# Optimization experiments

Hardware: AMD Instinct MI355X
Metric: run time of the kernel (lower is better)

## Reference

```python
import jax, jax.numpy as jnp
import numpy as np

DIM = 1024
NUM_HEADS = 16
HEAD_DIM = DIM // NUM_HEADS
EPS = 1e-6


def rmsnorm(x, scale):
    # normalize over last dim (head_dim)
    ms = jnp.mean(x * x, axis=-1, keepdims=True)
    return scale * (x * jax.lax.rsqrt(ms + EPS))


def setup_inputs() -> dict:
    key = jax.random.key(0)
    ks = jax.random.split(key, 12)
    B, Nx, Nc = 2, 2048, 256
    std = 1.0 / np.sqrt(DIM)
    return {
        "x": jax.random.normal(ks[0], (B, Nx, DIM), jnp.float32),
        "c": jax.random.normal(ks[1], (B, Nc, DIM), jnp.float32),
        "w_qkv_x": jax.random.normal(ks[2], (DIM, 3 * DIM), jnp.float32) * std,
        "b_qkv_x": jnp.zeros((3 * DIM,), jnp.float32),
        "w_qkv_c": jax.random.normal(ks[3], (DIM, 3 * DIM), jnp.float32) * std,
        "b_qkv_c": jnp.zeros((3 * DIM,), jnp.float32),
        "s_q_x": jnp.ones((HEAD_DIM,), jnp.float32),
        "s_k_x": jnp.ones((HEAD_DIM,), jnp.float32),
        "s_q_c": jnp.ones((HEAD_DIM,), jnp.float32),
        "s_k_c": jnp.ones((HEAD_DIM,), jnp.float32),
        "w_proj_x": jax.random.normal(ks[4], (DIM, DIM), jnp.float32) * std,
        "b_proj_x": jnp.zeros((DIM,), jnp.float32),
        "w_proj_c": jax.random.normal(ks[5], (DIM, DIM), jnp.float32) * std,
        "b_proj_c": jnp.zeros((DIM,), jnp.float32),
    }


def reference(x, c, w_qkv_x, b_qkv_x, w_qkv_c, b_qkv_c,
              s_q_x, s_k_x, s_q_c, s_k_c,
              w_proj_x, b_proj_x, w_proj_c, b_proj_c):
    B, Nx, C = x.shape
    Nc = c.shape[1]
    H, D = NUM_HEADS, HEAD_DIM

    def split_qkv(t, w, b, n):
        qkv = (t @ w + b).reshape(B, n, 3, H, D)
        qkv = jnp.transpose(qkv, (2, 0, 3, 1, 4))  # [3, B, H, n, D]
        return qkv[0], qkv[1], qkv[2]

    q_x, k_x, v_x = split_qkv(x, w_qkv_x, b_qkv_x, Nx)
    q_c, k_c, v_c = split_qkv(c, w_qkv_c, b_qkv_c, Nc)

    q = jnp.concatenate([rmsnorm(q_x, s_q_x), rmsnorm(q_c, s_q_c)], axis=2)
    k = jnp.concatenate([rmsnorm(k_x, s_k_x), rmsnorm(k_c, s_k_c)], axis=2)
    v = jnp.concatenate([v_x, v_c], axis=2)

    scale = 1.0 / jnp.sqrt(jnp.asarray(D, q.dtype))
    scores = jnp.einsum("bhqd,bhkd->bhqk", q, k) * scale
    attn = jax.nn.softmax(scores, axis=-1)
    out = jnp.einsum("bhqk,bhkd->bhqd", attn, v)  # [B, H, Nx+Nc, D]
    out = jnp.transpose(out, (0, 2, 1, 3)).reshape(B, Nx + Nc, C)

    x_out = out[:, :Nx] @ w_proj_x + b_proj_x
    c_out = out[:, Nx:] @ w_proj_c + b_proj_c
    return x_out, c_out
```

## Files before the change

kernel.cpp:

```cpp
#include <hip/hip_runtime.h>
#include <stdint.h>

typedef __attribute__((ext_vector_type(4))) float  f32x4;
typedef __attribute__((ext_vector_type(2))) float  f32x2;
typedef __attribute__((ext_vector_type(8))) short  s16x8;
typedef __attribute__((ext_vector_type(4))) short  s16x4;

constexpr int kDIM = 1024;
constexpr int kD   = 64;
constexpr int kNT  = 2304;

static __device__ __forceinline__ short f2bf(float f) {
  union { float f; uint32_t i; } x; x.f = f;
  uint32_t r = x.i + 0x7fffu + ((x.i >> 16) & 1u);
  return (short)(r >> 16);
}
static __device__ __forceinline__ uint32_t cvtpk(float lo, float hi) {
  uint32_t r;
  asm volatile("v_cvt_pk_bf16_f32 %0, %1, %2" : "=v"(r) : "v"(lo), "v"(hi));
  return r;
}
static __device__ __forceinline__ void gll16(const short* g, short* l) {
  __builtin_amdgcn_global_load_lds((const __attribute__((address_space(1))) void*)g,
                                   (__attribute__((address_space(3))) void*)l, 16, 0, 0);
}
#define FENCE() asm volatile("" ::: "memory")
#define WAITV8() asm volatile("s_waitcnt vmcnt(8)" ::: "memory")
#define WAITV2() asm volatile("s_waitcnt vmcnt(2)" ::: "memory")
#define WAITV0() asm volatile("s_waitcnt vmcnt(0)" ::: "memory")
#define WAITLGKM() do { asm volatile("s_waitcnt lgkmcnt(0)" ::: "memory"); \
                        __builtin_amdgcn_sched_barrier(0); } while (0)

__global__ __launch_bounds__(256) void k_cast2(const float* __restrict__ x,
                                               short* __restrict__ xb,
                                               const float* __restrict__ c,
                                               short* __restrict__ cb, int nxb) {
  int b = blockIdx.x;
  const float* in = x; short* out = xb;
  if (b >= nxb) { in = c; out = cb; b -= nxb; }
  int i = (b * 256 + threadIdx.x) * 4;
  f32x4 v = *(const f32x4*)(in + i);
  s16x4 o; o[0] = f2bf(v[0]); o[1] = f2bf(v[1]); o[2] = f2bf(v[2]); o[3] = f2bf(v[3]);
  *(s16x4*)(out + i) = o;
}

__global__ __launch_bounds__(256) void k_tcast2(const float* __restrict__ W0,
                                                short* __restrict__ Wt0,
                                                const float* __restrict__ W1,
                                                short* __restrict__ Wt1,
                                                int K, int N) {
  const float* W = blockIdx.z ? W1 : W0;
  short* Wt = blockIdx.z ? Wt1 : Wt0;
  __shared__ float tile[32][33];
  int n0 = blockIdx.x * 32, k0 = blockIdx.y * 32;
  int tx = threadIdx.x, ty = threadIdx.y;
#pragma unroll
  for (int i2 = 0; i2 < 4; ++i2) {
    int r = ty + 8 * i2;
    tile[r][tx] = W[(size_t)(k0 + r) * N + n0 + tx];
  }
  __syncthreads();
#pragma unroll
  for (int i2 = 0; i2 < 4; ++i2) {
    int r = ty + 8 * i2;
    Wt[(size_t)(n0 + r) * K + k0 + tx] = f2bf(tile[tx][r]);
  }
}

__global__ __launch_bounds__(256, 2) void k_gemm(
    const short* A0, const short* Wt0, const float* bias0,
    const float* sq0, const float* sk0,
    const short* A1, const short* Wt1, const float* bias1,
    const float* sq1, const float* sk1,
    short* outq, short* outk, short* outvt,
    float* outp0, float* outp1,
    int rpbs0, int arstride0, int aoff0, int posoff0,
    int rpbs1, int arstride1, int aoff1, int posoff1,
    int ybreak, int epi, int nx) {
  __shared__ __align__(16) short SH[32768];
  short* As0 = SH;          short* As1 = SH + 8192;
  short* Bs0 = SH + 16384;  short* Bs1 = SH + 24576;
  const int t = threadIdx.x;
  const int lane = t & 63, w = t >> 6;
  const int g = lane >> 4, r15 = lane & 15;
  const int wm = w >> 1, wn = w & 1;

  int lin = blockIdx.x;
  int xcd = lin & 7, kk = lin >> 3;
  int by = (xcd & 3) * 9 + kk % 9;
  int bx = (xcd >> 2) * (nx >> 1) + kk / 9;

  const short* A; const short* Wt; const float* bias;
  const float* sq; const float* sk; float* outp;
  int rpbs, arstride, aoff, posoff, my;
  if (by < ybreak) {
    A = A0; Wt = Wt0; bias = bias0; sq = sq0; sk = sk0; outp = outp0;
    rpbs = rpbs0; arstride = arstride0; aoff = aoff0; posoff = posoff0; my = by;
  } else {
    A = A1; Wt = Wt1; bias = bias1; sq = sq1; sk = sk1; outp = outp1;
    rpbs = rpbs1; arstride = arstride1; aoff = aoff1; posoff = posoff1; my = by - ybreak;
  }
  const int m0 = my * 128, n0 = bx * 128;

  const short* aptr[4]; const short* bptr[4];
  int wofs[4];
#pragma unroll
  for (int it = 0; it < 4; ++it) {
    int slot = t + 256 * it;
    int row = slot >> 3, gp = slot & 7;
    int gl = gp ^ (row & 7);
    int i = m0 + row;
    int arow = (i >> rpbs) * arstride + aoff + (i & ((1 << rpbs) - 1));
    aptr[it] = A + (size_t)arow * kDIM + 8 * gl;
    bptr[it] = Wt + (size_t)(n0 + row) * kDIM + 8 * gl;
    wofs[it] = (256 * it + 64 * w) * 8;
  }

  f32x4 acc[4][4] = {};

  auto STAGE = [&](short* Asd, short* Bsd) {
#pragma unroll
    for (int it = 0; it < 4; ++it) {
      gll16(aptr[it], Asd + wofs[it]);
      gll16(bptr[it], Bsd + wofs[it]);
      aptr[it] += 64; bptr[it] += 64;
    }
  };

  auto kstep = [&](const short* Ab, const short* Bb, short* Asd, short* Bsd,
                   bool last, bool pref) {
    if (last) WAITV0(); else WAITV8();
    __builtin_amdgcn_s_barrier();
    FENCE();
#pragma unroll
    for (int ks = 0; ks < 2; ++ks) {
      s16x8 af[4], bfr[4];
#pragma unroll
      for (int mf = 0; mf < 4; ++mf) {
        int row = wm * 64 + mf * 16 + r15;
        af[mf] = *(const s16x8*)(Ab + row * 64 + (((g + 4 * ks) ^ (row & 7)) * 8));
      }
#pragma unroll
      for (int nf = 0; nf < 4; ++nf) {
        int row = wn * 64 + nf * 16 + r15;
        bfr[nf] = *(const s16x8*)(Bb + row * 64 + (((g + 4 * ks) ^ (row & 7)) * 8));
      }
#pragma unroll
      for (int mf = 0; mf < 4; ++mf)
#pragma unroll
        for (int nf = 0; nf < 4; ++nf)
          acc[mf][nf] = __builtin_amdgcn_mfma_f32_16x16x32_bf16(af[mf], bfr[nf], acc[mf][nf], 0, 0, 0);
    }
    FENCE();
    __builtin_amdgcn_s_barrier();
    FENCE();
    if (pref) STAGE(Asd, Bsd);
  };

  STAGE(As0, Bs0);
  STAGE(As1, Bs1);
  for (int pp = 0; pp < 8; ++pp) {
    kstep(As0, Bs0, As0, Bs0, false,   pp < 7);
    kstep(As1, Bs1, As1, Bs1, pp == 7, pp < 7);
  }

  const int rpbm = (1 << rpbs) - 1;
  float* Ep = (float*)SH + w * 4096;

  if (epi == 1) {
#pragma unroll
    for (int mf = 0; mf < 4; ++mf)
#pragma unroll
      for (int nf = 0; nf < 4; ++nf) {
        f32x4 v = acc[mf][nf];
        float bj = bias[n0 + wn * 64 + nf * 16 + r15];
        int dl = nf * 16 + r15;
#pragma unroll
        for (int rg = 0; rg < 4; ++rg) {
          int r = mf * 16 + 4 * g + rg;
          Ep[r * 64 + (dl ^ ((r & 15) << 1))] = v[rg] + bj;
        }
      }
    WAITLGKM();
#pragma unroll
    for (int p2 = 0; p2 < 16; ++p2) {
      int r = 4 * p2 + (lane >> 4);
      int ch = lane & 15;
      int i = m0 + wm * 64 + r;
      f32x2 a = *(const f32x2*)&Ep[r * 64 + ((ch * 4) ^ ((r & 15) << 1))];
      f32x2 b2 = *(const f32x2*)&Ep[r * 64 + ((ch * 4 + 2) ^ ((r & 15) << 1))];
      f32x4 o; o[0] = a[0]; o[1] = a[1]; o[2] = b2[0]; o[3] = b2[1];
      *(f32x4*)(outp + (size_t)i * 1024 + n0 + wn * 64 + ch * 4) = o;
    }
    return;
  }

  const int eblk = (n0 + wn * 64) >> 10;
  const int hh = ((n0 + wn * 64) >> 6) & 15;
  if (eblk == 2) {
#pragma unroll
    for (int mf = 0; mf < 4; ++mf)
#pragma unroll
      for (int nf = 0; nf < 4; ++nf) {
        f32x4 v = acc[mf][nf];
        float bj = bias[n0 + wn * 64 + nf * 16 + r15];
        int dl = nf * 16 + r15;
#pragma unroll
        for (int rg = 0; rg < 4; ++rg) {
          int pin = mf * 16 + 4 * g + rg;
          int pp2 = (pin & 32) | (((pin >> 2) & 3) << 3) |
                    (((pin >> 4) & 1) << 2) | (pin & 3);
          Ep[dl * 64 + (pp2 ^ ((dl & 15) << 1))] = v[rg] + bj;
        }
      }
    WAITLGKM();
    int i0 = m0 + wm * 64;
    int b = i0 >> rpbs;
    int posb = (i0 & rpbm) + posoff;
#pragma unroll
    for (int p2 = 0; p2 < 8; ++p2) {
      int dl = 8 * p2 + (lane >> 3);
      int ch = lane & 7;
      union { uint32_t u[4]; s16x8 v; } o;
#pragma unroll
      for (int j = 0; j < 4; ++j) {
        f32x2 rd = *(const f32x2*)&Ep[dl * 64 + ((ch * 8 + 2 * j) ^ ((dl & 15) << 1))];
        o.u[j] = cvtpk(rd[0], rd[1]);
      }
      *(s16x8*)(outvt + ((size_t)((b * 16 + hh) * 64 + dl)) * kNT + posb + ch * 8) = o.v;
    }
  } else {
    const float* sv = (eblk == 0) ? sq : sk;
    short* dstb = (eblk == 0) ? outq : outk;
    const float post = (eblk == 0) ? 0.125f * 1.44269504f : 1.0f;
    float sl[4], bj4[4];
#pragma unroll
    for (int nf = 0; nf < 4; ++nf) {
      bj4[nf] = bias[n0 + wn * 64 + nf * 16 + r15];
      sl[nf] = sv[nf * 16 + r15] * post;
    }
#pragma unroll
    for (int mf = 0; mf < 4; ++mf) {
      float vb[4][4];
#pragma unroll
      for (int nf = 0; nf < 4; ++nf)
#pragma unroll
        for (int rg = 0; rg < 4; ++rg)
          vb[nf][rg] = acc[mf][nf][rg] + bj4[nf];
#pragma unroll
      for (int rg = 0; rg < 4; ++rg) {
        float ss = vb[0][rg] * vb[0][rg];
        ss = __builtin_fmaf(vb[1][rg], vb[1][rg], ss);
        ss = __builtin_fmaf(vb[2][rg], vb[2][rg], ss);
        ss = __builtin_fmaf(vb[3][rg], vb[3][rg], ss);
        ss += __shfl_xor(ss, 1); ss += __shfl_xor(ss, 2);
        ss += __shfl_xor(ss, 4); ss += __shfl_xor(ss, 8);
        float f = rsqrtf(ss * (1.f / 64.f) + 1e-6f);
        int r = mf * 16 + 4 * g + rg;
#pragma unroll
        for (int nf = 0; nf < 4; ++nf) {
          int dl = nf * 16 + r15;
          Ep[r * 64 + (dl ^ ((r & 15) << 1))] = vb[nf][rg] * f * sl[nf];
        }
      }
    }
    WAITLGKM();
#pragma unroll
    for (int p2 = 0; p2 < 8; ++p2) {
      int r = 8 * p2 + (lane >> 3);
      int ch = lane & 7;
      int i = m0 + wm * 64 + r;
      int b = i >> rpbs;
      int pos = (i & rpbm) + posoff;
      union { uint32_t u[4]; s16x8 v; } o;
#pragma unroll
      for (int j = 0; j < 4; ++j) {
        f32x2 rd = *(const f32x2*)&Ep[r * 64 + ((ch * 8 + 2 * j) ^ ((r & 15) << 1))];
        o.u[j] = cvtpk(rd[0], rd[1]);
      }
      *(s16x8*)(dstb + ((size_t)((b * 16 + hh) * kNT + pos)) * 64 + ch * 8) = o.v;
    }
  }
}

__global__ __launch_bounds__(512, 4) void k_attn(
    const short* __restrict__ Q, const short* __restrict__ K,
    const short* __restrict__ Vt, short* __restrict__ Ao) {
  __shared__ __align__(16) short S[16384];
  const int t = threadIdx.x;
  const int lane = t & 63, w = t >> 6;
  const int g = lane >> 4, r15 = lane & 15;
  const int lin = blockIdx.x;
  const int idx = lin >> 3;
  const int bh = (lin & 7) * 4 + idx / 18;
  const int q0 = (idx % 18) * 128;

  const short* qrow = Q + ((size_t)bh * kNT + q0 + 16 * w + r15) * kD;
  s16x8 qf0 = *(const s16x8*)(qrow + 8 * g);
  s16x8 qf1 = *(const s16x8*)(qrow + 32 + 8 * g);

  {
  }
  int srow = t >> 3, sgp = t & 7;
  int sgl = sgp ^ (srow & 7);
  const short* kptr = K + ((size_t)bh * kNT + srow) * kD + 8 * sgl;
  const short* vptr = Vt + ((size_t)bh * kD + srow) * kNT + 8 * sgl;
  const int sb2 = 512 * w;

  int ko[2][4], vo[2][4];
#pragma unroll
  for (int a = 0; a < 2; ++a)
#pragma unroll
    for (int rf = 0; rf < 4; ++rf) {
      int row = 16 * rf + r15;
      ko[a][rf] = row * 64 + (((g + 4 * a) ^ (row & 7)) * 8);
      vo[a][rf] = row * 64 + (((4 * a + g) ^ (row & 7)) * 8);
    }

  s16x8 onesf;
#pragma unroll
  for (int j = 0; j < 8; ++j) onesf[j] = (short)0x3F80;

  f32x4 ot[4] = {};
  f32x4 ls = {};
  short* Kb0 = S;          short* Kb1 = S + 4096;
  short* Vb0 = S + 8192;   short* Vb1 = S + 12288;

  auto STAGE = [&](short* kst, short* vst) {
    gll16(kptr, kst + sb2); kptr += 64 * kD;
    gll16(vptr, vst + sb2); vptr += 64;
  };

  auto tile = [&](const short* Kb, const short* Vb, short* kst, short* vst,
                  bool last, bool pref) {
    if (last) WAITV0(); else WAITV2();
    __builtin_amdgcn_s_barrier();
    FENCE();
    f32x4 st[4] = {};
    __builtin_amdgcn_s_setprio(1);
#pragma unroll
    for (int a = 0; a < 2; ++a) {
      s16x8 qk = a ? qf1 : qf0;
#pragma unroll
      for (int rf = 0; rf < 4; ++rf) {
        s16x8 kf = *(const s16x8*)(Kb + ko[a][rf]);
        st[rf] = __builtin_amdgcn_mfma_f32_16x16x32_bf16(kf, qk, st[rf], 0, 0, 0);
      }
    }
    __builtin_amdgcn_s_setprio(0);
    float pv[4][4];
#pragma unroll
    for (int rf = 0; rf < 4; ++rf)
#pragma unroll
      for (int j = 0; j < 4; ++j)
        pv[rf][j] = __builtin_amdgcn_exp2f(st[rf][j]);
    s16x8 pf[2];
#pragma unroll
    for (int c = 0; c < 2; ++c) {
      union { uint32_t u[4]; s16x8 v; } pk;
      pk.u[0] = cvtpk(pv[2 * c][0], pv[2 * c][1]);
      pk.u[1] = cvtpk(pv[2 * c][2], pv[2 * c][3]);
      pk.u[2] = cvtpk(pv[2 * c + 1][0], pv[2 * c + 1][1]);
      pk.u[3] = cvtpk(pv[2 * c + 1][2], pv[2 * c + 1][3]);
      pf[c] = pk.v;
    }
    __builtin_amdgcn_s_setprio(1);
#pragma unroll
    for (int mf = 0; mf < 4; ++mf)
#pragma unroll
      for (int c = 0; c < 2; ++c) {
        s16x8 vf = *(const s16x8*)(Vb + vo[c][mf]);
        ot[mf] = __builtin_amdgcn_mfma_f32_16x16x32_bf16(vf, pf[c], ot[mf], 0, 0, 0);
      }
#pragma unroll
    for (int c = 0; c < 2; ++c)
      ls = __builtin_amdgcn_mfma_f32_16x16x32_bf16(onesf, pf[c], ls, 0, 0, 0);
    __builtin_amdgcn_s_setprio(0);
    FENCE();
    __builtin_amdgcn_s_barrier();
    FENCE();
    if (pref) STAGE(kst, vst);
  };

  STAGE(Kb0, Vb0);
  STAGE(Kb1, Vb1);
  for (int pp = 0; pp < 18; ++pp) {
    tile(Kb0, Vb0, Kb0, Vb0, false,    pp < 17);
    tile(Kb1, Vb1, Kb1, Vb1, pp == 17, pp < 17);
  }

  float rl = 1.f / ls[0];

  __syncthreads();
  float* Os = (float*)S;
#pragma unroll
  for (int mf = 0; mf < 4; ++mf)
#pragma unroll
    for (int rg = 0; rg < 4; ++rg) {
      int d = 16 * mf + 4 * g + rg;
      int R = 16 * w + r15;
      Os[R * 64 + (d ^ ((r15 & 7) << 3))] = ot[mf][rg] * rl;
    }
  __syncthreads();
  {
    int b = bh >> 4, h = bh & 15;
    int q = t >> 2, c4 = t & 3;
    float vals[16];
#pragma unroll
    for (int i = 0; i < 4; ++i) {
      f32x4 rd = *(const f32x4*)&Os[q * 64 + (((c4 * 16 + 4 * i) ^ ((q & 7) << 3)))];
      vals[4 * i + 0] = rd[0]; vals[4 * i + 1] = rd[1];
      vals[4 * i + 2] = rd[2]; vals[4 * i + 3] = rd[3];
    }
    union { uint32_t u[4]; s16x8 v; } o0, o1;
    o0.u[0] = cvtpk(vals[0], vals[1]);   o0.u[1] = cvtpk(vals[2], vals[3]);
    o0.u[2] = cvtpk(vals[4], vals[5]);   o0.u[3] = cvtpk(vals[6], vals[7]);
    o1.u[0] = cvtpk(vals[8], vals[9]);   o1.u[1] = cvtpk(vals[10], vals[11]);
    o1.u[2] = cvtpk(vals[12], vals[13]); o1.u[3] = cvtpk(vals[14], vals[15]);
    short* dst = Ao + ((size_t)b * kNT + q0 + q) * kDIM + h * kD + c4 * 16;
    *(s16x8*)dst = o0.v;
    *(s16x8*)(dst + 8) = o1.v;
  }
}

extern "C" void kernel_launch(void* const* d_in, const int* in_sizes, int n_in,
                              void* d_out, int out_size, void* d_ws, size_t ws_size,
                              hipStream_t stream) {
  const float* x   = (const float*)d_in[0];
  const float* c   = (const float*)d_in[1];
  const float* wqx = (const float*)d_in[2];
  const float* bqx = (const float*)d_in[3];
  const float* wqc = (const float*)d_in[4];
  const float* bqc = (const float*)d_in[5];
  const float* sqx = (const float*)d_in[6];
  const float* skx = (const float*)d_in[7];
  const float* sqc = (const float*)d_in[8];
  const float* skc = (const float*)d_in[9];
  const float* wpx = (const float*)d_in[10];
  const float* bpx = (const float*)d_in[11];
  const float* wpc = (const float*)d_in[12];
  const float* bpc = (const float*)d_in[13];
  float* out = (float*)d_out;

  char* p = (char*)d_ws;
  short* xb   = (short*)p; p += (size_t)4096 * 1024 * 2;
  short* cb   = (short*)p; p += (size_t)512 * 1024 * 2;
  short* wqxt = (short*)p; p += (size_t)3072 * 1024 * 2;
  short* wqct = (short*)p; p += (size_t)3072 * 1024 * 2;
  short* wpxt = (short*)p; p += (size_t)1024 * 1024 * 2;
  short* wpct = (short*)p; p += (size_t)1024 * 1024 * 2;
  short* qb   = (short*)p; p += (size_t)32 * 2304 * 64 * 2;
  short* kb   = (short*)p; p += (size_t)32 * 2304 * 64 * 2;
  short* vtb  = (short*)p; p += (size_t)32 * 64 * 2304 * 2;
  short* ao   = (short*)p; p += (size_t)2 * 2304 * 1024 * 2;

  k_cast2<<<4608, 256, 0, stream>>>(x, xb, c, cb, 4096);
  k_tcast2<<<dim3(96, 32, 2), dim3(32, 8), 0, stream>>>(wqx, wqxt, wqc, wqct, 1024, 3072);
  k_tcast2<<<dim3(32, 32, 2), dim3(32, 8), 0, stream>>>(wpx, wpxt, wpc, wpct, 1024, 1024);

  k_gemm<<<864, 256, 0, stream>>>(
      xb, wqxt, bqx, sqx, skx,
      cb, wqct, bqc, sqc, skc,
      qb, kb, vtb, nullptr, nullptr,
      11, 2048, 0, 0,
      8, 256, 0, 2048,
      32, 0, 24);

  k_attn<<<576, 512, 0, stream>>>(qb, kb, vtb, ao);

  k_gemm<<<288, 256, 0, stream>>>(
      ao, wpxt, bpx, nullptr, nullptr,
      ao, wpct, bpc, nullptr, nullptr,
      nullptr, nullptr, nullptr, out, out + (size_t)4096 * 1024,
      11, 2304, 0, 0,
      8, 2304, 2048, 0,
      32, 1, 8);
}
```

Measured before the change: 130.1 us.

## Give each attention wave four query fragments and shrink blocks to two waves

The attention kernel now runs 128-thread blocks where each wave handles 64 query rows (four 16-row fragments) instead of 16. Each K/V fragment read from shared memory is reused across four MFMAs, and the staging loop issues four loads per thread to fill the same tiles. This cuts LDS traffic per MFMA and barrier overhead per unit of work. In exchange it raises register pressure from the larger accumulators and leaves far fewer waves per CU to hide latency. The vmcnt wait is adjusted to match the larger number of in-flight loads.

```diff
diff --git a/kernel.cpp b/kernel.cpp
--- a/kernel.cpp
+++ b/kernel.cpp
@@ -26,7 +26,6 @@
 }
 #define FENCE() asm volatile("" ::: "memory")
 #define WAITV8() asm volatile("s_waitcnt vmcnt(8)" ::: "memory")
-#define WAITV2() asm volatile("s_waitcnt vmcnt(2)" ::: "memory")
 #define WAITV0() asm volatile("s_waitcnt vmcnt(0)" ::: "memory")
 #define WAITLGKM() do { asm volatile("s_waitcnt lgkmcnt(0)" ::: "memory"); \
                         __builtin_amdgcn_sched_barrier(0); } while (0)
@@ -283,7 +282,7 @@
   }
 }
 
-__global__ __launch_bounds__(512, 4) void k_attn(
+__global__ __launch_bounds__(128, 2) void k_attn(
     const short* __restrict__ Q, const short* __restrict__ K,
     const short* __restrict__ Vt, short* __restrict__ Ao) {
   __shared__ __align__(16) short S[16384];
@@ -295,17 +294,25 @@
   const int bh = (lin & 7) * 4 + idx / 18;
   const int q0 = (idx % 18) * 128;
 
-  const short* qrow = Q + ((size_t)bh * kNT + q0 + 16 * w + r15) * kD;
-  s16x8 qf0 = *(const s16x8*)(qrow + 8 * g);
-  s16x8 qf1 = *(const s16x8*)(qrow + 32 + 8 * g);
-
-  {
-  }
-  int srow = t >> 3, sgp = t & 7;
-  int sgl = sgp ^ (srow & 7);
-  const short* kptr = K + ((size_t)bh * kNT + srow) * kD + 8 * sgl;
-  const short* vptr = Vt + ((size_t)bh * kD + srow) * kNT + 8 * sgl;
-  const int sb2 = 512 * w;
+  s16x8 qf[4][2];
+#pragma unroll
+  for (int qi = 0; qi < 4; ++qi) {
+    const short* qrow = Q + ((size_t)bh * kNT + q0 + 64 * w + 16 * qi + r15) * kD;
+    qf[qi][0] = *(const s16x8*)(qrow + 8 * g);
+    qf[qi][1] = *(const s16x8*)(qrow + 32 + 8 * g);
+  }
+
+  const short* kptr[4]; const short* vptr[4];
+  int sb[4];
+#pragma unroll
+  for (int it = 0; it < 4; ++it) {
+    int slot = lane + 64 * (2 * it + w);
+    int row = slot >> 3, gp = slot & 7;
+    int gl = gp ^ (row & 7);
+    kptr[it] = K + ((size_t)bh * kNT + row) * kD + 8 * gl;
+    vptr[it] = Vt + ((size_t)bh * kD + row) * kNT + 8 * gl;
+    sb[it] = 512 * (2 * it + w);
+  }
 
   int ko[2][4], vo[2][4];
 #pragma unroll
@@ -321,60 +328,72 @@
 #pragma unroll
   for (int j = 0; j < 8; ++j) onesf[j] = (short)0x3F80;
 
-  f32x4 ot[4] = {};
-  f32x4 ls = {};
+  f32x4 ot[4][4] = {};
+  f32x4 ls[4] = {};
   short* Kb0 = S;          short* Kb1 = S + 4096;
   short* Vb0 = S + 8192;   short* Vb1 = S + 12288;
 
   auto STAGE = [&](short* kst, short* vst) {
-    gll16(kptr, kst + sb2); kptr += 64 * kD;
-    gll16(vptr, vst + sb2); vptr += 64;
+#pragma unroll
+    for (int it = 0; it < 4; ++it) {
+      gll16(kptr[it], kst + sb[it]); kptr[it] += 64 * kD;
+      gll16(vptr[it], vst + sb[it]); vptr[it] += 64;
+    }
   };
 
   auto tile = [&](const short* Kb, const short* Vb, short* kst, short* vst,
                   bool last, bool pref) {
-    if (last) WAITV0(); else WAITV2();
+    if (last) WAITV0(); else WAITV8();
     __builtin_amdgcn_s_barrier();
     FENCE();
-    f32x4 st[4] = {};
+    f32x4 st[4][4];
     __builtin_amdgcn_s_setprio(1);
 #pragma unroll
-    for (int a = 0; a < 2; ++a) {
-      s16x8 qk = a ? qf1 : qf0;
+    for (int a = 0; a < 2; ++a)
 #pragma unroll
       for (int rf = 0; rf < 4; ++rf) {
         s16x8 kf = *(const s16x8*)(Kb + ko[a][rf]);
-        st[rf] = __builtin_amdgcn_mfma_f32_16x16x32_bf16(kf, qk, st[rf], 0, 0, 0);
-      }
-    }
+#pragma unroll
+        for (int qi = 0; qi < 4; ++qi) {
+          if (a == 0) st[qi][rf] = __builtin_amdgcn_mfma_f32_16x16x32_bf16(kf, qf[qi][0], f32x4{}, 0, 0, 0);
+          else        st[qi][rf] = __builtin_amdgcn_mfma_f32_16x16x32_bf16(kf, qf[qi][1], st[qi][rf], 0, 0, 0);
+        }
+      }
     __builtin_amdgcn_s_setprio(0);
-    float pv[4][4];
-#pragma unroll
-    for (int rf = 0; rf < 4; ++rf)
-#pragma unroll
-      for (int j = 0; j < 4; ++j)
-        pv[rf][j] = __builtin_amdgcn_exp2f(st[rf][j]);
-    s16x8 pf[2];
-#pragma unroll
-    for (int c = 0; c < 2; ++c) {
-      union { uint32_t u[4]; s16x8 v; } pk;
-      pk.u[0] = cvtpk(pv[2 * c][0], pv[2 * c][1]);
-      pk.u[1] = cvtpk(pv[2 * c][2], pv[2 * c][3]);
-      pk.u[2] = cvtpk(pv[2 * c + 1][0], pv[2 * c + 1][1]);
-      pk.u[3] = cvtpk(pv[2 * c + 1][2], pv[2 * c + 1][3]);
-      pf[c] = pk.v;
+    s16x8 pf[4][2];
+#pragma unroll
+    for (int qi = 0; qi < 4; ++qi) {
+      float pv[4][4];
+#pragma unroll
+      for (int rf = 0; rf < 4; ++rf)
+#pragma unroll
+        for (int j = 0; j < 4; ++j)
+          pv[rf][j] = __builtin_amdgcn_exp2f(st[qi][rf][j]);
+#pragma unroll
+      for (int c = 0; c < 2; ++c) {
+        union { uint32_t u[4]; s16x8 v; } pk;
+        pk.u[0] = cvtpk(pv[2 * c][0], pv[2 * c][1]);
+        pk.u[1] = cvtpk(pv[2 * c][2], pv[2 * c][3]);
+        pk.u[2] = cvtpk(pv[2 * c + 1][0], pv[2 * c + 1][1]);
+        pk.u[3] = cvtpk(pv[2 * c + 1][2], pv[2 * c + 1][3]);
+        pf[qi][c] = pk.v;
+      }
     }
     __builtin_amdgcn_s_setprio(1);
 #pragma unroll
-    for (int mf = 0; mf < 4; ++mf)
-#pragma unroll
-      for (int c = 0; c < 2; ++c) {
+    for (int c = 0; c < 2; ++c)
+#pragma unroll
+      for (int mf = 0; mf < 4; ++mf) {
         s16x8 vf = *(const s16x8*)(Vb + vo[c][mf]);
-        ot[mf] = __builtin_amdgcn_mfma_f32_16x16x32_bf16(vf, pf[c], ot[mf], 0, 0, 0);
+#pragma unroll
+        for (int qi = 0; qi < 4; ++qi)
+          ot[qi][mf] = __builtin_amdgcn_mfma_f32_16x16x32_bf16(vf, pf[qi][c], ot[qi][mf], 0, 0, 0);
       }
 #pragma unroll
     for (int c = 0; c < 2; ++c)
-      ls = __builtin_amdgcn_mfma_f32_16x16x32_bf16(onesf, pf[c], ls, 0, 0, 0);
+#pragma unroll
+      for (int qi = 0; qi < 4; ++qi)
+        ls[qi] = __builtin_amdgcn_mfma_f32_16x16x32_bf16(onesf, pf[qi][c], ls[qi], 0, 0, 0);
     __builtin_amdgcn_s_setprio(0);
     FENCE();
     __builtin_amdgcn_s_barrier();
@@ -389,37 +408,45 @@
     tile(Kb1, Vb1, Kb1, Vb1, pp == 17, pp < 17);
   }
 
-  float rl = 1.f / ls[0];
+  float rl[4];
+#pragma unroll
+  for (int qi = 0; qi < 4; ++qi) rl[qi] = 1.f / ls[qi][0];
 
   __syncthreads();
   float* Os = (float*)S;
 #pragma unroll
-  for (int mf = 0; mf < 4; ++mf)
-#pragma unroll
-    for (int rg = 0; rg < 4; ++rg) {
-      int d = 16 * mf + 4 * g + rg;
-      int R = 16 * w + r15;
-      Os[R * 64 + (d ^ ((r15 & 7) << 3))] = ot[mf][rg] * rl;
-    }
+  for (int qi = 0; qi < 4; ++qi)
+#pragma unroll
+    for (int mf = 0; mf < 4; ++mf)
+#pragma unroll
+      for (int rg = 0; rg < 4; ++rg) {
+        int d = 16 * mf + 4 * g + rg;
+        int R = 64 * w + 16 * qi + r15;
+        Os[R * 64 + (d ^ ((r15 & 7) << 3))] = ot[qi][mf][rg] * rl[qi];
+      }
   __syncthreads();
   {
     int b = bh >> 4, h = bh & 15;
-    int q = t >> 2, c4 = t & 3;
-    float vals[16];
-#pragma unroll
-    for (int i = 0; i < 4; ++i) {
-      f32x4 rd = *(const f32x4*)&Os[q * 64 + (((c4 * 16 + 4 * i) ^ ((q & 7) << 3)))];
-      vals[4 * i + 0] = rd[0]; vals[4 * i + 1] = rd[1];
-      vals[4 * i + 2] = rd[2]; vals[4 * i + 3] = rd[3];
-    }
-    union { uint32_t u[4]; s16x8 v; } o0, o1;
-    o0.u[0] = cvtpk(vals[0], vals[1]);   o0.u[1] = cvtpk(vals[2], vals[3]);
-    o0.u[2] = cvtpk(vals[4], vals[5]);   o0.u[3] = cvtpk(vals[6], vals[7]);
-    o1.u[0] = cvtpk(vals[8], vals[9]);   o1.u[1] = cvtpk(vals[10], vals[11]);
-    o1.u[2] = cvtpk(vals[12], vals[13]); o1.u[3] = cvtpk(vals[14], vals[15]);
-    short* dst = Ao + ((size_t)b * kNT + q0 + q) * kDIM + h * kD + c4 * 16;
-    *(s16x8*)dst = o0.v;
-    *(s16x8*)(dst + 8) = o1.v;
+#pragma unroll
+    for (int rep = 0; rep < 4; ++rep) {
+      int idx2 = t + 128 * rep;
+      int q = idx2 >> 2, c4 = idx2 & 3;
+      float vals[16];
+#pragma unroll
+      for (int i = 0; i < 4; ++i) {
+        f32x4 rd = *(const f32x4*)&Os[q * 64 + (((c4 * 16 + 4 * i) ^ ((q & 7) << 3)))];
+        vals[4 * i + 0] = rd[0]; vals[4 * i + 1] = rd[1];
+        vals[4 * i + 2] = rd[2]; vals[4 * i + 3] = rd[3];
+      }
+      union { uint32_t u[4]; s16x8 v; } o0, o1;
+      o0.u[0] = cvtpk(vals[0], vals[1]);   o0.u[1] = cvtpk(vals[2], vals[3]);
+      o0.u[2] = cvtpk(vals[4], vals[5]);   o0.u[3] = cvtpk(vals[6], vals[7]);
+      o1.u[0] = cvtpk(vals[8], vals[9]);   o1.u[1] = cvtpk(vals[10], vals[11]);
+      o1.u[2] = cvtpk(vals[12], vals[13]); o1.u[3] = cvtpk(vals[14], vals[15]);
+      short* dst = Ao + ((size_t)b * kNT + q0 + q) * kDIM + h * kD + c4 * 16;
+      *(s16x8*)dst = o0.v;
+      *(s16x8*)(dst + 8) = o1.v;
+    }
   }
 }
 
@@ -466,7 +493,7 @@
       8, 256, 0, 2048,
       32, 0, 24);
 
-  k_attn<<<576, 512, 0, stream>>>(qb, kb, vtb, ao);
+  k_attn<<<576, 128, 0, stream>>>(qb, kb, vtb, ao);
 
   k_gemm<<<288, 256, 0, stream>>>(
       ao, wpxt, bpx, nullptr, nullptr,
```

Result: slower. 138.3 us (+6.2%).

## Switch attention kernel to 32x32x16 MFMA with 256-thread blocks

Applied to the files above, without the earlier changes.

Rewrites the attention inner loop to use 32x32x16 bf16 MFMA instructions, with each wave owning 32 query rows, and halves the block to 256 threads, so each thread now stages two K/V chunks per tile. The row sum is now built with scalar adds plus a cross-lane shuffle, replacing the extra ones-vector MFMA. The bit permutation in the GEMM epilogue is also simplified. The aim is fewer MFMA issues and LDS fragment reads per unit of work, at the cost of larger accumulator register use and fewer waves per block to hide latency.

```diff
diff --git a/kernel.cpp b/kernel.cpp
--- a/kernel.cpp
+++ b/kernel.cpp
@@ -1,10 +1,11 @@
 #include <hip/hip_runtime.h>
 #include <stdint.h>
 
-typedef __attribute__((ext_vector_type(4))) float  f32x4;
-typedef __attribute__((ext_vector_type(2))) float  f32x2;
-typedef __attribute__((ext_vector_type(8))) short  s16x8;
-typedef __attribute__((ext_vector_type(4))) short  s16x4;
+typedef __attribute__((ext_vector_type(4)))  float f32x4;
+typedef __attribute__((ext_vector_type(2)))  float f32x2;
+typedef __attribute__((ext_vector_type(16))) float f32x16;
+typedef __attribute__((ext_vector_type(8)))  short s16x8;
+typedef __attribute__((ext_vector_type(4)))  short s16x4;
 
 constexpr int kDIM = 1024;
 constexpr int kD   = 64;
@@ -26,7 +27,7 @@
 }
 #define FENCE() asm volatile("" ::: "memory")
 #define WAITV8() asm volatile("s_waitcnt vmcnt(8)" ::: "memory")
-#define WAITV2() asm volatile("s_waitcnt vmcnt(2)" ::: "memory")
+#define WAITV4() asm volatile("s_waitcnt vmcnt(4)" ::: "memory")
 #define WAITV0() asm volatile("s_waitcnt vmcnt(0)" ::: "memory")
 #define WAITLGKM() do { asm volatile("s_waitcnt lgkmcnt(0)" ::: "memory"); \
                         __builtin_amdgcn_sched_barrier(0); } while (0)
@@ -208,8 +209,7 @@
 #pragma unroll
         for (int rg = 0; rg < 4; ++rg) {
           int pin = mf * 16 + 4 * g + rg;
-          int pp2 = (pin & 32) | (((pin >> 2) & 3) << 3) |
-                    (((pin >> 4) & 1) << 2) | (pin & 3);
+          int pp2 = (pin & 51) | ((pin & 4) << 1) | ((pin & 8) >> 1);
           Ep[dl * 64 + (pp2 ^ ((dl & 15) << 1))] = v[rg] + bj;
         }
       }
@@ -283,98 +283,104 @@
   }
 }
 
-__global__ __launch_bounds__(512, 4) void k_attn(
+__global__ __launch_bounds__(256, 3) void k_attn(
     const short* __restrict__ Q, const short* __restrict__ K,
     const short* __restrict__ Vt, short* __restrict__ Ao) {
   __shared__ __align__(16) short S[16384];
   const int t = threadIdx.x;
   const int lane = t & 63, w = t >> 6;
-  const int g = lane >> 4, r15 = lane & 15;
+  const int h = lane >> 5, q31 = lane & 31;
   const int lin = blockIdx.x;
   const int idx = lin >> 3;
   const int bh = (lin & 7) * 4 + idx / 18;
   const int q0 = (idx % 18) * 128;
 
-  const short* qrow = Q + ((size_t)bh * kNT + q0 + 16 * w + r15) * kD;
-  s16x8 qf0 = *(const s16x8*)(qrow + 8 * g);
-  s16x8 qf1 = *(const s16x8*)(qrow + 32 + 8 * g);
-
-  {
-  }
-  int srow = t >> 3, sgp = t & 7;
-  int sgl = sgp ^ (srow & 7);
-  const short* kptr = K + ((size_t)bh * kNT + srow) * kD + 8 * sgl;
-  const short* vptr = Vt + ((size_t)bh * kD + srow) * kNT + 8 * sgl;
-  const int sb2 = 512 * w;
+  const short* qrow = Q + ((size_t)bh * kNT + q0 + 32 * w + q31) * kD;
+  s16x8 qf[4];
+#pragma unroll
+  for (int a = 0; a < 4; ++a)
+    qf[a] = *(const s16x8*)(qrow + 16 * a + 8 * h);
+
+  const short* kptr[2]; const short* vptr[2];
+  int sb[2];
+#pragma unroll
+  for (int it = 0; it < 2; ++it) {
+    int slot = t + 256 * it;
+    int row = slot >> 3, gp = slot & 7;
+    int gl = gp ^ (row & 7);
+    kptr[it] = K + ((size_t)bh * kNT + row) * kD + 8 * gl;
+    vptr[it] = Vt + ((size_t)bh * kD + row) * kNT + 8 * gl;
+    sb[it] = (256 * it + 64 * w) * 8;
+  }
 
   int ko[2][4], vo[2][4];
 #pragma unroll
-  for (int a = 0; a < 2; ++a)
-#pragma unroll
-    for (int rf = 0; rf < 4; ++rf) {
-      int row = 16 * rf + r15;
-      ko[a][rf] = row * 64 + (((g + 4 * a) ^ (row & 7)) * 8);
-      vo[a][rf] = row * 64 + (((4 * a + g) ^ (row & 7)) * 8);
-    }
-
-  s16x8 onesf;
-#pragma unroll
-  for (int j = 0; j < 8; ++j) onesf[j] = (short)0x3F80;
-
-  f32x4 ot[4] = {};
-  f32x4 ls = {};
+  for (int rg = 0; rg < 2; ++rg) {
+    int row = 32 * rg + q31;
+#pragma unroll
+    for (int a = 0; a < 4; ++a) {
+      ko[rg][a] = row * 64 + (((2 * a + h) ^ (row & 7)) * 8);
+      vo[rg][a] = ko[rg][a];
+    }
+  }
+
+  f32x16 ot0 = {}, ot1 = {};
+  float l = 0.f;
   short* Kb0 = S;          short* Kb1 = S + 4096;
   short* Vb0 = S + 8192;   short* Vb1 = S + 12288;
 
   auto STAGE = [&](short* kst, short* vst) {
-    gll16(kptr, kst + sb2); kptr += 64 * kD;
-    gll16(vptr, vst + sb2); vptr += 64;
+#pragma unroll
+    for (int it = 0; it < 2; ++it) {
+      gll16(kptr[it], kst + sb[it]); kptr[it] += 64 * kD;
+      gll16(vptr[it], vst + sb[it]); vptr[it] += 64;
+    }
   };
 
   auto tile = [&](const short* Kb, const short* Vb, short* kst, short* vst,
                   bool last, bool pref) {
-    if (last) WAITV0(); else WAITV2();
+    if (last) WAITV0(); else WAITV4();
     __builtin_amdgcn_s_barrier();
     FENCE();
-    f32x4 st[4] = {};
+    f32x16 st0 = {}, st1 = {};
     __builtin_amdgcn_s_setprio(1);
 #pragma unroll
-    for (int a = 0; a < 2; ++a) {
-      s16x8 qk = a ? qf1 : qf0;
-#pragma unroll
-      for (int rf = 0; rf < 4; ++rf) {
-        s16x8 kf = *(const s16x8*)(Kb + ko[a][rf]);
-        st[rf] = __builtin_amdgcn_mfma_f32_16x16x32_bf16(kf, qk, st[rf], 0, 0, 0);
-      }
+    for (int a = 0; a < 4; ++a) {
+      s16x8 kf0 = *(const s16x8*)(Kb + ko[0][a]);
+      s16x8 kf1 = *(const s16x8*)(Kb + ko[1][a]);
+      st0 = __builtin_amdgcn_mfma_f32_32x32x16_bf16(kf0, qf[a], st0, 0, 0, 0);
+      st1 = __builtin_amdgcn_mfma_f32_32x32x16_bf16(kf1, qf[a], st1, 0, 0, 0);
     }
     __builtin_amdgcn_s_setprio(0);
-    float pv[4][4];
-#pragma unroll
-    for (int rf = 0; rf < 4; ++rf)
-#pragma unroll
-      for (int j = 0; j < 4; ++j)
-        pv[rf][j] = __builtin_amdgcn_exp2f(st[rf][j]);
-    s16x8 pf[2];
-#pragma unroll
-    for (int c = 0; c < 2; ++c) {
-      union { uint32_t u[4]; s16x8 v; } pk;
-      pk.u[0] = cvtpk(pv[2 * c][0], pv[2 * c][1]);
-      pk.u[1] = cvtpk(pv[2 * c][2], pv[2 * c][3]);
-      pk.u[2] = cvtpk(pv[2 * c + 1][0], pv[2 * c + 1][1]);
-      pk.u[3] = cvtpk(pv[2 * c + 1][2], pv[2 * c + 1][3]);
-      pf[c] = pk.v;
-    }
+    s16x8 pf[4];
+    float rs = 0.f;
+#pragma unroll
+    for (int rg = 0; rg < 2; ++rg) {
+      float p[16];
+#pragma unroll
+      for (int r = 0; r < 16; ++r) {
+        p[r] = __builtin_amdgcn_exp2f(rg ? st1[r] : st0[r]);
+        rs += p[r];
+      }
+#pragma unroll
+      for (int mh = 0; mh < 2; ++mh) {
+        union { uint32_t u[4]; s16x8 v; } pk;
+        pk.u[0] = cvtpk(p[8 * mh + 0], p[8 * mh + 1]);
+        pk.u[1] = cvtpk(p[8 * mh + 2], p[8 * mh + 3]);
+        pk.u[2] = cvtpk(p[8 * mh + 4], p[8 * mh + 5]);
+        pk.u[3] = cvtpk(p[8 * mh + 6], p[8 * mh + 7]);
+        pf[2 * rg + mh] = pk.v;
+      }
+    }
+    l += rs;
     __builtin_amdgcn_s_setprio(1);
 #pragma unroll
-    for (int mf = 0; mf < 4; ++mf)
-#pragma unroll
-      for (int c = 0; c < 2; ++c) {
-        s16x8 vf = *(const s16x8*)(Vb + vo[c][mf]);
-        ot[mf] = __builtin_amdgcn_mfma_f32_16x16x32_bf16(vf, pf[c], ot[mf], 0, 0, 0);
-      }
-#pragma unroll
-    for (int c = 0; c < 2; ++c)
-      ls = __builtin_amdgcn_mfma_f32_16x16x32_bf16(onesf, pf[c], ls, 0, 0, 0);
+    for (int m = 0; m < 4; ++m) {
+      s16x8 vf0 = *(const s16x8*)(Vb + vo[0][m]);
+      s16x8 vf1 = *(const s16x8*)(Vb + vo[1][m]);
+      ot0 = __builtin_amdgcn_mfma_f32_32x32x16_bf16(vf0, pf[m], ot0, 0, 0, 0);
+      ot1 = __builtin_amdgcn_mfma_f32_32x32x16_bf16(vf1, pf[m], ot1, 0, 0, 0);
+    }
     __builtin_amdgcn_s_setprio(0);
     FENCE();
     __builtin_amdgcn_s_barrier();
@@ -389,37 +395,46 @@
     tile(Kb1, Vb1, Kb1, Vb1, pp == 17, pp < 17);
   }
 
-  float rl = 1.f / ls[0];
+  l += __shfl_xor(l, 32);
+  float rl = 1.f / l;
 
   __syncthreads();
   float* Os = (float*)S;
-#pragma unroll
-  for (int mf = 0; mf < 4; ++mf)
-#pragma unroll
-    for (int rg = 0; rg < 4; ++rg) {
-      int d = 16 * mf + 4 * g + rg;
-      int R = 16 * w + r15;
-      Os[R * 64 + (d ^ ((r15 & 7) << 3))] = ot[mf][rg] * rl;
+  const int R = 32 * w + q31;
+#pragma unroll
+  for (int rg = 0; rg < 2; ++rg)
+#pragma unroll
+    for (int rr = 0; rr < 4; ++rr) {
+      int d0 = 32 * rg + 8 * rr + 4 * h;
+      f32x4 v4;
+#pragma unroll
+      for (int j = 0; j < 4; ++j)
+        v4[j] = (rg ? ot1[4 * rr + j] : ot0[4 * rr + j]) * rl;
+      *(f32x4*)&Os[R * 64 + (d0 ^ ((R & 7) << 3))] = v4;
     }
   __syncthreads();
   {
-    int b = bh >> 4, h = bh & 15;
-    int q = t >> 2, c4 = t & 3;
-    float vals[16];
-#pragma unroll
-    for (int i = 0; i < 4; ++i) {
-      f32x4 rd = *(const f32x4*)&Os[q * 64 + (((c4 * 16 + 4 * i) ^ ((q & 7) << 3)))];
-      vals[4 * i + 0] = rd[0]; vals[4 * i + 1] = rd[1];
-      vals[4 * i + 2] = rd[2]; vals[4 * i + 3] = rd[3];
-    }
-    union { uint32_t u[4]; s16x8 v; } o0, o1;
-    o0.u[0] = cvtpk(vals[0], vals[1]);   o0.u[1] = cvtpk(vals[2], vals[3]);
-    o0.u[2] = cvtpk(vals[4], vals[5]);   o0.u[3] = cvtpk(vals[6], vals[7]);
-    o1.u[0] = cvtpk(vals[8], vals[9]);   o1.u[1] = cvtpk(vals[10], vals[11]);
-    o1.u[2] = cvtpk(vals[12], vals[13]); o1.u[3] = cvtpk(vals[14], vals[15]);
-    short* dst = Ao + ((size_t)b * kNT + q0 + q) * kDIM + h * kD + c4 * 16;
-    *(s16x8*)dst = o0.v;
-    *(s16x8*)(dst + 8) = o1.v;
+    int b = bh >> 4, hh = bh & 15;
+#pragma unroll
+    for (int rep = 0; rep < 2; ++rep) {
+      int idx2 = t + 256 * rep;
+      int q = idx2 >> 2, c4 = idx2 & 3;
+      float vals[16];
+#pragma unroll
+      for (int i = 0; i < 4; ++i) {
+        f32x4 rd = *(const f32x4*)&Os[q * 64 + (((c4 * 16 + 4 * i) ^ ((q & 7) << 3)))];
+        vals[4 * i + 0] = rd[0]; vals[4 * i + 1] = rd[1];
+        vals[4 * i + 2] = rd[2]; vals[4 * i + 3] = rd[3];
+      }
+      union { uint32_t u[4]; s16x8 v; } o0, o1;
+      o0.u[0] = cvtpk(vals[0], vals[1]);   o0.u[1] = cvtpk(vals[2], vals[3]);
+      o0.u[2] = cvtpk(vals[4], vals[5]);   o0.u[3] = cvtpk(vals[6], vals[7]);
+      o1.u[0] = cvtpk(vals[8], vals[9]);   o1.u[1] = cvtpk(vals[10], vals[11]);
+      o1.u[2] = cvtpk(vals[12], vals[13]); o1.u[3] = cvtpk(vals[14], vals[15]);
+      short* dst = Ao + ((size_t)b * kNT + q0 + q) * kDIM + hh * kD + c4 * 16;
+      *(s16x8*)dst = o0.v;
+      *(s16x8*)(dst + 8) = o1.v;
+    }
   }
 }
 
@@ -466,7 +481,7 @@
       8, 256, 0, 2048,
       32, 0, 24);
 
-  k_attn<<<576, 512, 0, stream>>>(qb, kb, vtb, ao);
+  k_attn<<<576, 256, 0, stream>>>(qb, kb, vtb, ao);
 
   k_gemm<<<288, 256, 0, stream>>>(
       ao, wpxt, bpx, nullptr, nullptr,
```

Result: slower. 139.3 us (+7.1%).
